# Performance work log

Hardware: AMD Instinct MI355X
Metric: run time of the kernel (lower is better)

The kernel has to match this reference:

```python
import math
import jax, jax.numpy as jnp
import numpy as np

IN_SIZE = 16
OUT_SIZE = 16
MIN_SCALE = 1e-3
CONST = 1000.0
DEFAULT_U_A = math.log(math.e - 1.0 - MIN_SCALE)
BATCH = 32768
N_PARAMS = OUT_SIZE ** 2 + 2 * OUT_SIZE + OUT_SIZE * IN_SIZE  # 544


def setup_inputs() -> dict:
    key = jax.random.key(0)
    kx, kh = jax.random.split(key)
    x = jax.random.normal(kx, (BATCH, IN_SIZE), dtype=jnp.float32)
    h = jax.random.normal(kh, (BATCH, N_PARAMS), dtype=jnp.float32)
    return {"x": x, "h": h}


def reference(x, h):
    B = h.shape[0]
    O, I = OUT_SIZE, IN_SIZE
    # extract_parameters
    da = h[:, :O]                                   # (B,O)
    db = h[:, O:2 * O]                              # (B,O)
    dw = h[:, 2 * O:2 * O + O * O].reshape(B, O, O)  # (B,O,O)
    du = h[:, 2 * O + O * O:].reshape(B, O, I)       # (B,O,I)

    u_pre = du / CONST
    u = jax.nn.softmax(u_pre, axis=-1)
    log_u = jax.nn.log_softmax(u_pre, axis=-1)
    a = jax.nn.softplus(DEFAULT_U_A + da / CONST) + MIN_SCALE
    b = db / CONST
    w_pre = dw / CONST
    w = jax.nn.softmax(w_pre, axis=-1)
    log_w = jax.nn.log_softmax(w_pre, axis=-1)

    # forward transform
    ux = jnp.einsum('boi,bi->bo', u, x)             # (B,O)
    c = jax.nn.sigmoid(a * ux + b)                  # (B,O)
    d = jnp.einsum('bij,bj->bi', w, c)              # (B,O)
    z = jnp.log(d / (1.0 - d))                      # inverse_sigmoid

    # log-space Jacobian: J = diag(1/(d(1-d))) @ W @ diag(sigma'(c)*a) @ U
    log_t1 = (jnp.log(d) - jnp.log(1.0 - d))[:, :, None]                  # (B,O,1)
    log_t3 = (jax.nn.log_sigmoid(c) + jax.nn.log_sigmoid(-c))[:, None, :]  # (B,1,O)
    log_t4 = jnp.log(a)[:, None, :]                                        # (B,1,O)
    m1 = (log_t1 + log_w + log_t3 + log_t4)[:, :, :, None]                 # (B,O,O,1)
    m2 = log_u[:, None, :, :]                                              # (B,1,O,I)
    # log_dot: logsumexp over the contraction dim (-2), keepdim
    log_jac = jax.scipy.special.logsumexp(m1 + m2, axis=-2, keepdims=True)  # (B,O,1,I)
    log_det = jnp.sum(log_jac, axis=(1, 2, 3))                              # (B,)
    return z, log_det


if __name__ == "__main__":
    out = reference(**setup_inputs())
    print(out[0].shape, out[1].shape)
```

## Files before the change

### kernel.cpp

```cpp
#include <hip/hip_runtime.h>

#define BATCH 32768
#define EPB   16
#define RS    20
#define US    328
#define CS    40

__device__ __forceinline__ float pexp1k(float v) {
    float t = v * 1.0e-3f;
    return 1.0f + t * (1.0f + t * (0.5f + t * 0.16666667f));
}

__global__ __launch_bounds__(256, 4)
void dsit_kernel(const float* __restrict__ x, const float* __restrict__ h,
                 float* __restrict__ out_z, float* __restrict__ out_ld) {
    __shared__ float u_s[EPB * US];
    __shared__ float cs_s[EPB * CS];

    const int tid = threadIdx.x;
    const int blk = blockIdx.x;
    const int e = tid >> 4;
    const int r = tid & 15;

    const float* hb = h + (size_t)blk * (EPB * 544) + e * 544;

    float x_val = x[(size_t)blk * 256 + tid];
    float da = hb[r];
    float db = hb[16 + r];

    float ur[16], wr[16];
    *(float4*)&ur[0]  = *(const float4*)(hb + 288 + 16 * r);
    *(float4*)&ur[4]  = *(const float4*)(hb + 288 + 16 * r + 4);
    *(float4*)&ur[8]  = *(const float4*)(hb + 288 + 16 * r + 8);
    *(float4*)&ur[12] = *(const float4*)(hb + 288 + 16 * r + 12);
    *(float4*)&wr[0]  = *(const float4*)(hb + 32 + 16 * r);
    *(float4*)&wr[4]  = *(const float4*)(hb + 32 + 16 * r + 4);
    *(float4*)&wr[8]  = *(const float4*)(hb + 32 + 16 * r + 8);
    *(float4*)&wr[12] = *(const float4*)(hb + 32 + 16 * r + 12);

    float usum = 0.0f;
    #pragma unroll
    for (int i = 0; i < 16; ++i) { ur[i] = pexp1k(ur[i]); usum += ur[i]; }
    float uinv = 1.0f / usum;

    float dot = 0.0f;
    #pragma unroll
    for (int i = 0; i < 16; ++i) dot += ur[i] * __shfl(x_val, i, 16);
    float ux = uinv * dot;

    #pragma unroll
    for (int q = 0; q < 4; ++q) {
        float4 t = make_float4(ur[4*q] * uinv, ur[4*q+1] * uinv,
                               ur[4*q+2] * uinv, ur[4*q+3] * uinv);
        *(float4*)&u_s[e * US + r * RS + 4 * q] = t;
    }

    float wsum = 0.0f;
    #pragma unroll
    for (int j = 0; j < 16; ++j) { wr[j] = pexp1k(wr[j]); wsum += wr[j]; }
    float winv = 1.0f / wsum;
    #pragma unroll
    for (int j = 0; j < 16; ++j) wr[j] *= winv;

    float ta = da * 1.0e-3f;
    float a  = 1.0006320f + ta * (0.6319822f + 0.1162903f * ta);
    float bb = db * 1.0e-3f;

    float cpre = fmaf(a, ux, bb);
    float c  = 1.0f / (1.0f + __expf(-cpre));
    float sc = 1.0f / (1.0f + __expf(-c));
    float s  = sc * (1.0f - sc) * a;
    *(float2*)&cs_s[e * CS + 2 * r] = make_float2(c, s);

    float d = 0.0f;
    #pragma unroll
    for (int j = 0; j < 16; ++j) {
        float2 cs = *(const float2*)&cs_s[e * CS + 2 * j];
        d = fmaf(wr[j], cs.x, d);
        wr[j] *= cs.y;
    }
    float z = __logf(d / (1.0f - d));
    out_z[(size_t)blk * 256 + tid] = z;

    float part = 16.0f * z;
    float prod = 1.0f;
    #pragma unroll
    for (int i4 = 0; i4 < 4; ++i4) {
        float ax = 0.f, ay = 0.f, az = 0.f, aw = 0.f;
        #pragma unroll
        for (int j = 0; j < 16; ++j) {
            float wj = wr[j];
            float4 uq = *(const float4*)&u_s[e * US + j * RS + (i4 << 2)];
            ax = fmaf(wj, uq.x, ax); ay = fmaf(wj, uq.y, ay);
            az = fmaf(wj, uq.z, az); aw = fmaf(wj, uq.w, aw);
        }
        prod *= (ax * ay) * (az * aw);
        if (i4 == 1) { part += __logf(prod); prod = 1.0f; }
    }
    part += __logf(prod);

    #pragma unroll
    for (int m = 1; m < 16; m <<= 1) part += __shfl_xor(part, m, 16);
    if (r == 0) out_ld[blk * EPB + e] = part;
}

extern "C" void kernel_launch(void* const* d_in, const int* in_sizes, int n_in,
                              void* d_out, int out_size, void* d_ws, size_t ws_size,
                              hipStream_t stream) {
    const float* x = (const float*)d_in[0];
    const float* h = (const float*)d_in[1];
    float* out_z  = (float*)d_out;
    float* out_ld = out_z + (size_t)BATCH * 16;

    dsit_kernel<<<dim3(BATCH / EPB), dim3(256), 0, stream>>>(x, h, out_z, out_ld);
}
```

Measured before the change: 100.2 us.

## Compute two output rows per thread to reuse shared-memory U loads

Each thread now handles two output rows of one batch element, using 8 threads per element and 32 elements per block instead of 16 threads per element and 16 elements per block. Each float4 of U read from LDS and each (c, s) pair now feeds two rows of FMAs, which roughly halves LDS traffic per FMA in the Jacobian and d loops. The x vector is staged through shared memory instead of being broadcast with shuffles. In exchange, registers per thread roughly double and the launch-bounds occupancy hint drops from 4 to 3 blocks, so there are fewer resident waves to hide latency.

```diff
diff --git a/kernel.cpp b/kernel.cpp
--- a/kernel.cpp
+++ b/kernel.cpp
@@ -1,107 +1,137 @@
 #include <hip/hip_runtime.h>
 
 #define BATCH 32768
-#define EPB   16
+#define EPB   32
 #define RS    20
-#define US    328
-#define CS    40
+#define US    324
+#define CS    38
+#define XS    18
 
 __device__ __forceinline__ float pexp1k(float v) {
     float t = v * 1.0e-3f;
     return 1.0f + t * (1.0f + t * (0.5f + t * 0.16666667f));
 }
 
-__global__ __launch_bounds__(256, 4)
+__global__ __launch_bounds__(256, 3)
 void dsit_kernel(const float* __restrict__ x, const float* __restrict__ h,
                  float* __restrict__ out_z, float* __restrict__ out_ld) {
     __shared__ float u_s[EPB * US];
     __shared__ float cs_s[EPB * CS];
+    __shared__ float x_s[EPB * XS];
 
     const int tid = threadIdx.x;
     const int blk = blockIdx.x;
-    const int e = tid >> 4;
-    const int r = tid & 15;
+    const int e = tid >> 3;
+    const int q = tid & 7;
 
     const float* hb = h + (size_t)blk * (EPB * 544) + e * 544;
 
-    float x_val = x[(size_t)blk * 256 + tid];
-    float da = hb[r];
-    float db = hb[16 + r];
+    float2 xv = *(const float2*)(x + (size_t)blk * (EPB * 16) + e * 16 + 2 * q);
+    *(float2*)&x_s[e * XS + 2 * q] = xv;
 
-    float ur[16], wr[16];
-    *(float4*)&ur[0]  = *(const float4*)(hb + 288 + 16 * r);
-    *(float4*)&ur[4]  = *(const float4*)(hb + 288 + 16 * r + 4);
-    *(float4*)&ur[8]  = *(const float4*)(hb + 288 + 16 * r + 8);
-    *(float4*)&ur[12] = *(const float4*)(hb + 288 + 16 * r + 12);
-    *(float4*)&wr[0]  = *(const float4*)(hb + 32 + 16 * r);
-    *(float4*)&wr[4]  = *(const float4*)(hb + 32 + 16 * r + 4);
-    *(float4*)&wr[8]  = *(const float4*)(hb + 32 + 16 * r + 8);
-    *(float4*)&wr[12] = *(const float4*)(hb + 32 + 16 * r + 12);
+    float daA = hb[q],      daB = hb[q + 8];
+    float dbA = hb[16 + q], dbB = hb[24 + q];
 
-    float usum = 0.0f;
+    float uA[16], uB[16], wA[16], wB[16];
     #pragma unroll
-    for (int i = 0; i < 16; ++i) { ur[i] = pexp1k(ur[i]); usum += ur[i]; }
-    float uinv = 1.0f / usum;
+    for (int k = 0; k < 4; ++k) {
+        *(float4*)&uA[4 * k] = *(const float4*)(hb + 288 + 16 * q + 4 * k);
+        *(float4*)&uB[4 * k] = *(const float4*)(hb + 288 + 16 * (q + 8) + 4 * k);
+        *(float4*)&wA[4 * k] = *(const float4*)(hb + 32 + 16 * q + 4 * k);
+        *(float4*)&wB[4 * k] = *(const float4*)(hb + 32 + 16 * (q + 8) + 4 * k);
+    }
 
-    float dot = 0.0f;
+    float sA = 0.f, sB = 0.f;
     #pragma unroll
-    for (int i = 0; i < 16; ++i) dot += ur[i] * __shfl(x_val, i, 16);
-    float ux = uinv * dot;
+    for (int i = 0; i < 16; ++i) {
+        uA[i] = pexp1k(uA[i]); sA += uA[i];
+        uB[i] = pexp1k(uB[i]); sB += uB[i];
+    }
+    float uinvA = 1.0f / sA, uinvB = 1.0f / sB;
+
+    float dotA = 0.f, dotB = 0.f;
+    #pragma unroll
+    for (int i2 = 0; i2 < 8; ++i2) {
+        float2 xx = *(const float2*)&x_s[e * XS + 2 * i2];
+        dotA = fmaf(uA[2 * i2], xx.x, fmaf(uA[2 * i2 + 1], xx.y, dotA));
+        dotB = fmaf(uB[2 * i2], xx.x, fmaf(uB[2 * i2 + 1], xx.y, dotB));
+    }
+    float uxA = dotA * uinvA, uxB = dotB * uinvB;
 
     #pragma unroll
-    for (int q = 0; q < 4; ++q) {
-        float4 t = make_float4(ur[4*q] * uinv, ur[4*q+1] * uinv,
-                               ur[4*q+2] * uinv, ur[4*q+3] * uinv);
-        *(float4*)&u_s[e * US + r * RS + 4 * q] = t;
+    for (int k = 0; k < 4; ++k) {
+        float4 ta = make_float4(uA[4*k] * uinvA, uA[4*k+1] * uinvA,
+                                uA[4*k+2] * uinvA, uA[4*k+3] * uinvA);
+        float4 tb = make_float4(uB[4*k] * uinvB, uB[4*k+1] * uinvB,
+                                uB[4*k+2] * uinvB, uB[4*k+3] * uinvB);
+        *(float4*)&u_s[e * US + q * RS + 4 * k]       = ta;
+        *(float4*)&u_s[e * US + (q + 8) * RS + 4 * k] = tb;
     }
 
-    float wsum = 0.0f;
+    float twA = 0.f, twB = 0.f;
     #pragma unroll
-    for (int j = 0; j < 16; ++j) { wr[j] = pexp1k(wr[j]); wsum += wr[j]; }
-    float winv = 1.0f / wsum;
+    for (int j = 0; j < 16; ++j) {
+        wA[j] = pexp1k(wA[j]); twA += wA[j];
+        wB[j] = pexp1k(wB[j]); twB += wB[j];
+    }
+    float winvA = 1.0f / twA, winvB = 1.0f / twB;
     #pragma unroll
-    for (int j = 0; j < 16; ++j) wr[j] *= winv;
+    for (int j = 0; j < 16; ++j) { wA[j] *= winvA; wB[j] *= winvB; }
 
-    float ta = da * 1.0e-3f;
-    float a  = 1.0006320f + ta * (0.6319822f + 0.1162903f * ta);
-    float bb = db * 1.0e-3f;
+    float taA = daA * 1.0e-3f, taB = daB * 1.0e-3f;
+    float aA = 1.0006320f + taA * (0.6319822f + 0.1162903f * taA);
+    float aB = 1.0006320f + taB * (0.6319822f + 0.1162903f * taB);
+    float bbA = dbA * 1.0e-3f, bbB = dbB * 1.0e-3f;
 
-    float cpre = fmaf(a, ux, bb);
-    float c  = 1.0f / (1.0f + __expf(-cpre));
-    float sc = 1.0f / (1.0f + __expf(-c));
-    float s  = sc * (1.0f - sc) * a;
-    *(float2*)&cs_s[e * CS + 2 * r] = make_float2(c, s);
+    float cA = 1.0f / (1.0f + __expf(-fmaf(aA, uxA, bbA)));
+    float cB = 1.0f / (1.0f + __expf(-fmaf(aB, uxB, bbB)));
+    float scA = 1.0f / (1.0f + __expf(-cA));
+    float scB = 1.0f / (1.0f + __expf(-cB));
+    float ssA = scA * (1.0f - scA) * aA;
+    float ssB = scB * (1.0f - scB) * aB;
+    *(float2*)&cs_s[e * CS + 2 * q]        = make_float2(cA, ssA);
+    *(float2*)&cs_s[e * CS + 2 * (q + 8)]  = make_float2(cB, ssB);
 
-    float d = 0.0f;
+    float dA = 0.f, dB = 0.f;
     #pragma unroll
     for (int j = 0; j < 16; ++j) {
         float2 cs = *(const float2*)&cs_s[e * CS + 2 * j];
-        d = fmaf(wr[j], cs.x, d);
-        wr[j] *= cs.y;
+        dA = fmaf(wA[j], cs.x, dA);
+        dB = fmaf(wB[j], cs.x, dB);
+        wA[j] *= cs.y; wB[j] *= cs.y;
     }
-    float z = __logf(d / (1.0f - d));
-    out_z[(size_t)blk * 256 + tid] = z;
+    float zA = __logf(dA / (1.0f - dA));
+    float zB = __logf(dB / (1.0f - dB));
+    size_t zb = (size_t)blk * (EPB * 16) + e * 16;
+    out_z[zb + q]     = zA;
+    out_z[zb + q + 8] = zB;
 
-    float part = 16.0f * z;
-    float prod = 1.0f;
+    float part = 16.0f * (zA + zB);
+    float prodA = 1.0f, prodB = 1.0f;
     #pragma unroll
     for (int i4 = 0; i4 < 4; ++i4) {
-        float ax = 0.f, ay = 0.f, az = 0.f, aw = 0.f;
+        float a0=0.f,a1=0.f,a2=0.f,a3=0.f, b0=0.f,b1=0.f,b2=0.f,b3=0.f;
         #pragma unroll
         for (int j = 0; j < 16; ++j) {
-            float wj = wr[j];
             float4 uq = *(const float4*)&u_s[e * US + j * RS + (i4 << 2)];
-            ax = fmaf(wj, uq.x, ax); ay = fmaf(wj, uq.y, ay);
-            az = fmaf(wj, uq.z, az); aw = fmaf(wj, uq.w, aw);
+            float wa = wA[j], wb = wB[j];
+            a0 = fmaf(wa, uq.x, a0); a1 = fmaf(wa, uq.y, a1);
+            a2 = fmaf(wa, uq.z, a2); a3 = fmaf(wa, uq.w, a3);
+            b0 = fmaf(wb, uq.x, b0); b1 = fmaf(wb, uq.y, b1);
+            b2 = fmaf(wb, uq.z, b2); b3 = fmaf(wb, uq.w, b3);
         }
-        prod *= (ax * ay) * (az * aw);
-        if (i4 == 1) { part += __logf(prod); prod = 1.0f; }
+        prodA *= (a0 * a1) * (a2 * a3);
+        prodB *= (b0 * b1) * (b2 * b3);
+        if (i4 == 1) {
+            part += __logf(prodA) + __logf(prodB);
+            prodA = 1.0f; prodB = 1.0f;
+        }
     }
-    part += __logf(prod);
+    part += __logf(prodA) + __logf(prodB);
 
     #pragma unroll
-    for (int m = 1; m < 16; m <<= 1) part += __shfl_xor(part, m, 16);
-    if (r == 0) out_ld[blk * EPB + e] = part;
+    for (int m = 1; m < 8; m <<= 1) part += __shfl_xor(part, m, 8);
+    if (q == 0) out_ld[blk * EPB + e] = part;
 }
 
 extern "C" void kernel_launch(void* const* d_in, const int* in_sizes, int n_in,
```

Result: slower. 105.2 us (+5.0%).
